# Optimization experiments

Measured on AMD Instinct MI355X. Metric: run time of the kernel, lower is better.

Reference implementation:

```python
import jax, jax.numpy as jnp
import numpy as np

N_NODES = 50000
N_EDGES = 800000
DIM = 64
N_HEADS = 4


def setup_inputs() -> dict:
    key = jax.random.key(0)
    ks = jax.random.split(key, 7)
    x = jax.random.normal(ks[0], (N_NODES, DIM), dtype=jnp.float32)
    Wq = jax.random.normal(ks[1], (DIM, DIM), dtype=jnp.float32) / np.sqrt(DIM)
    Wk = jax.random.normal(ks[2], (DIM, DIM), dtype=jnp.float32) / np.sqrt(DIM)
    Wv = jax.random.normal(ks[3], (DIM, DIM), dtype=jnp.float32) / np.sqrt(DIM)
    Wo = jax.random.normal(ks[4], (DIM, DIM), dtype=jnp.float32) / np.sqrt(DIM)
    src = jax.random.randint(ks[5], (N_EDGES,), 0, N_NODES, dtype=jnp.int32)
    dst = jax.random.randint(ks[6], (N_EDGES,), 0, N_NODES, dtype=jnp.int32)
    return {"x": x, "Wq": Wq, "Wk": Wk, "Wv": Wv, "Wo": Wo, "src": src, "dst": dst}


def _scatter_softmax(scores, dst, n_nodes):
    # scores: [E, H]; per-destination-node softmax over incoming edges.
    m = jax.ops.segment_max(scores, dst, num_segments=n_nodes)  # [N, H]
    m = jnp.maximum(m, jnp.float32(-1e9))  # mirror the -1e9 init of the torch code
    ex = jnp.exp(scores - m[dst])  # [E, H]
    denom = jax.ops.segment_sum(ex, dst, num_segments=n_nodes)  # [N, H]
    return ex / (denom[dst] + 1e-9)


def reference(x, Wq, Wk, Wv, Wo, src, dst):
    N, D = x.shape
    H = N_HEADS
    Dh = D // H
    q = (x @ Wq).reshape(N, H, Dh)
    k = (x @ Wk).reshape(N, H, Dh)
    v = (x @ Wv).reshape(N, H, Dh)
    # per-edge attention logits: [E, H]
    scores = jnp.einsum("ehd,ehd->eh", q[dst], k[src]) / jnp.sqrt(jnp.float32(Dh))
    alpha = _scatter_softmax(scores, dst, N)  # [E, H]
    # weighted aggregation of source values onto destination nodes
    agg = jax.ops.segment_sum(alpha[:, :, None] * v[src], dst, num_segments=N)  # [N, H, Dh]
    return agg.reshape(N, D) @ Wo
```

## Files before the change

### kernel.cpp

```cpp
#include <hip/hip_runtime.h>
#include <math.h>

#define HEADS 4
#define DH 16
#define D 64
#define MAXDEG 64

typedef unsigned short ushort_t;
typedef unsigned int uint_t;

__device__ __forceinline__ float bf2f(ushort_t u) {
    return __uint_as_float(((uint_t)u) << 16);
}
__device__ __forceinline__ ushort_t f2bf(float f) {
    uint_t u = __float_as_uint(f);
    u = (u + 0x7FFFu + ((u >> 16) & 1u)) >> 16;
    return (ushort_t)u;
}
__device__ __forceinline__ float bflo(uint_t u) { return __uint_as_float(u << 16); }
__device__ __forceinline__ float bfhi(uint_t u) { return __uint_as_float(u & 0xFFFF0000u); }

__global__ __launch_bounds__(256) void scatter_qkv_kernel(
        const float* __restrict__ x,
        const float* __restrict__ Wq,
        const float* __restrict__ Wk,
        const float* __restrict__ Wv,
        ushort_t* __restrict__ qbf,
        ushort_t* __restrict__ kbf,
        ushort_t* __restrict__ vbf,
        const int* __restrict__ src,
        const int* __restrict__ dst,
        int* __restrict__ cursor,
        ushort_t* __restrict__ csr,
        int N, int E) {
    __shared__ ushort_t wq[D][D];
    __shared__ ushort_t wk[D][D];
    __shared__ ushort_t wv[D][D];
    __shared__ float xs[16][D];

    int tid = threadIdx.x;

    {
        int e0 = (int)((long long)E * blockIdx.x / gridDim.x);
        int e1 = (int)((long long)E * (blockIdx.x + 1) / gridDim.x);
        for (int e = e0 + tid; e < e1; e += 256) {
            int d = dst[e];
            int s = src[e];
            int pos = atomicAdd(&cursor[d], 1);
            if (pos < MAXDEG) csr[(size_t)d * MAXDEG + pos] = (ushort_t)s;
        }
    }

    for (int i = tid; i < D * D; i += 256) {
        wq[i >> 6][i & 63] = f2bf(Wq[i]);
        wk[i >> 6][i & 63] = f2bf(Wk[i]);
        wv[i >> 6][i & 63] = f2bf(Wv[i]);
    }

    int c = tid & 63;
    int g = tid >> 6;
    int row = tid >> 4;
    int col4 = tid & 15;

    int ntiles = (N + 15) >> 4;
    for (int tile = blockIdx.x; tile < ntiles; tile += gridDim.x) {
        int n0t = tile * 16;
        __syncthreads();
        float4 xv = make_float4(0.f, 0.f, 0.f, 0.f);
        if (n0t + row < N) xv = *(const float4*)(x + (size_t)(n0t + row) * D + col4 * 4);
        *(float4*)&xs[row][col4 * 4] = xv;
        __syncthreads();

        float aq0=0,aq1=0,aq2=0,aq3=0, ak0=0,ak1=0,ak2=0,ak3=0, av0=0,av1=0,av2=0,av3=0;
#pragma unroll 8
        for (int d = 0; d < D; ++d) {
            float wqv = bf2f(wq[d][c]), wkv = bf2f(wk[d][c]), wvv = bf2f(wv[d][c]);
            float x0 = xs[g*4+0][d], x1 = xs[g*4+1][d], x2 = xs[g*4+2][d], x3 = xs[g*4+3][d];
            aq0 += x0*wqv; ak0 += x0*wkv; av0 += x0*wvv;
            aq1 += x1*wqv; ak1 += x1*wkv; av1 += x1*wvv;
            aq2 += x2*wqv; ak2 += x2*wkv; av2 += x2*wvv;
            aq3 += x3*wqv; ak3 += x3*wkv; av3 += x3*wvv;
        }
        int nb = n0t + g * 4;
        if (nb+0 < N) { qbf[(size_t)(nb+0)*D+c]=f2bf(aq0); kbf[(size_t)(nb+0)*D+c]=f2bf(ak0); vbf[(size_t)(nb+0)*D+c]=f2bf(av0); }
        if (nb+1 < N) { qbf[(size_t)(nb+1)*D+c]=f2bf(aq1); kbf[(size_t)(nb+1)*D+c]=f2bf(ak1); vbf[(size_t)(nb+1)*D+c]=f2bf(av1); }
        if (nb+2 < N) { qbf[(size_t)(nb+2)*D+c]=f2bf(aq2); kbf[(size_t)(nb+2)*D+c]=f2bf(ak2); vbf[(size_t)(nb+2)*D+c]=f2bf(av2); }
        if (nb+3 < N) { qbf[(size_t)(nb+3)*D+c]=f2bf(aq3); kbf[(size_t)(nb+3)*D+c]=f2bf(ak3); vbf[(size_t)(nb+3)*D+c]=f2bf(av3); }
    }
}

__global__ __launch_bounds__(512) void attn_kernel(const ushort_t* __restrict__ qbf,
                                                   const ushort_t* __restrict__ kbf,
                                                   const ushort_t* __restrict__ vbf,
                                                   const ushort_t* __restrict__ csr,
                                                   const int* __restrict__ cursor,
                                                   const float* __restrict__ Wo,
                                                   float* __restrict__ out,
                                                   int N) {
    __shared__ float wo[D][D];
    __shared__ float aggsh[8][D];

    int tid = threadIdx.x;
    for (int i = tid; i < D * D; i += 512) wo[i >> 6][i & 63] = Wo[i];
    __syncthreads();

    int lane = tid & 63;
    int wave = tid >> 6;
    int node = blockIdx.x * 8 + wave;
    if (node >= N) return;

    int hp  = lane & 3;
    int el  = lane >> 2;
    int hd  = (lane & 31) >> 3;
    int par = lane >> 5;
    int dp2 = 2 * (lane & 31);

    int cnt = cursor[node]; if (cnt > MAXDEG) cnt = MAXDEG;
    const ushort_t* row = csr + (size_t)node * MAXDEG;

    float qr[16];
    {
        const uint4* qp = (const uint4*)(qbf + (size_t)node * D + hp * DH);
        uint4 qa = qp[0], qb = qp[1];
        qr[0]=bflo(qa.x);  qr[1]=bfhi(qa.x);  qr[2]=bflo(qa.y);  qr[3]=bfhi(qa.y);
        qr[4]=bflo(qa.z);  qr[5]=bfhi(qa.z);  qr[6]=bflo(qa.w);  qr[7]=bfhi(qa.w);
        qr[8]=bflo(qb.x);  qr[9]=bfhi(qb.x);  qr[10]=bflo(qb.y); qr[11]=bfhi(qb.y);
        qr[12]=bflo(qb.z); qr[13]=bfhi(qb.z); qr[14]=bflo(qb.w); qr[15]=bfhi(qb.w);
    }

    int s0=0, s1=0, s2=0, s3=0;
    float sc0=-1e30f, sc1=-1e30f, sc2=-1e30f, sc3=-1e30f;

#define PH1SB(sb, sv, scv)                                                      \
    if ((sb) * 16 < cnt) {                                                      \
        int eidx = (sb) * 16 + el;                                              \
        if (eidx < cnt) sv = row[eidx];                                         \
        const uint4* kp = (const uint4*)(kbf + (size_t)sv * D + hp * DH);       \
        uint4 ka = kp[0], kb = kp[1];                                           \
        float dot =                                                             \
          bflo(ka.x)*qr[0]  + bfhi(ka.x)*qr[1]                                  \
        + bflo(ka.y)*qr[2]  + bfhi(ka.y)*qr[3]                                  \
        + bflo(ka.z)*qr[4]  + bfhi(ka.z)*qr[5]                                  \
        + bflo(ka.w)*qr[6]  + bfhi(ka.w)*qr[7]                                  \
        + bflo(kb.x)*qr[8]  + bfhi(kb.x)*qr[9]                                  \
        + bflo(kb.y)*qr[10] + bfhi(kb.y)*qr[11]                                 \
        + bflo(kb.z)*qr[12] + bfhi(kb.z)*qr[13]                                 \
        + bflo(kb.w)*qr[14] + bfhi(kb.w)*qr[15];                                \
        scv = (eidx < cnt) ? dot * 0.25f : -1e30f;                              \
    }
    PH1SB(0, s0, sc0)
    PH1SB(1, s1, sc1)
    PH1SB(2, s2, sc2)
    PH1SB(3, s3, sc3)
#undef PH1SB

    float mloc = fmaxf(fmaxf(sc0, sc1), fmaxf(sc2, sc3));
    mloc = fmaxf(mloc, __shfl_xor(mloc, 4, 64));
    mloc = fmaxf(mloc, __shfl_xor(mloc, 8, 64));
    mloc = fmaxf(mloc, __shfl_xor(mloc, 16, 64));
    mloc = fmaxf(mloc, __shfl_xor(mloc, 32, 64));
    mloc = fmaxf(mloc, -1e9f);

    float pv0 = __expf(sc0 - mloc);
    float pv1 = __expf(sc1 - mloc);
    float pv2 = __expf(sc2 - mloc);
    float pv3 = __expf(sc3 - mloc);
    float ls = (pv0 + pv1) + (pv2 + pv3);
    ls += __shfl_xor(ls, 4, 64);
    ls += __shfl_xor(ls, 8, 64);
    ls += __shfl_xor(ls, 16, 64);
    ls += __shfl_xor(ls, 32, 64);

    float inv = 1.f / (__shfl(ls, hd, 64) + 1e-9f);

    float2 a0 = {0.f, 0.f}, a1 = {0.f, 0.f};
#define PH3SB(sb, sv, pvv)                                                      \
    if ((sb) * 16 < cnt) {                                                      \
        int lim = cnt - (sb) * 16; if (lim > 16) lim = 16;                      \
        for (int e2 = 0; e2 < lim; e2 += 4) {                                   \
            int L0 = 4 * (e2 + par);                                            \
            int ss0 = __shfl(sv, L0, 64);                                       \
            float p0 = __shfl(pvv, L0 + hd, 64);                                \
            uint_t w0 = *(const uint_t*)(vbf + (size_t)ss0 * D + dp2);          \
            a0.x += p0 * bflo(w0);                                              \
            a0.y += p0 * bfhi(w0);                                              \
            int L1 = 4 * (e2 + 2 + par);                                        \
            int ss1 = __shfl(sv, L1, 64);                                       \
            float p1 = __shfl(pvv, L1 + hd, 64);                                \
            uint_t w1 = *(const uint_t*)(vbf + (size_t)ss1 * D + dp2);          \
            a1.x += p1 * bflo(w1);                                              \
            a1.y += p1 * bfhi(w1);                                              \
        }                                                                       \
    }
    PH3SB(0, s0, pv0)
    PH3SB(1, s1, pv1)
    PH3SB(2, s2, pv2)
    PH3SB(3, s3, pv3)
#undef PH3SB

    float ax = a0.x + a1.x, ay = a0.y + a1.y;
    ax += __shfl_xor(ax, 32, 64);
    ay += __shfl_xor(ay, 32, 64);
    if (lane < 32) {
        aggsh[wave][dp2]     = ax * inv;
        aggsh[wave][dp2 + 1] = ay * inv;
    }

    float o = 0.f;
#pragma unroll 8
    for (int d = 0; d < D; ++d) {
        o += aggsh[wave][d] * wo[d][lane];
    }
    out[(size_t)node * D + lane] = o;
}

extern "C" void kernel_launch(void* const* d_in, const int* in_sizes, int n_in,
                              void* d_out, int out_size, void* d_ws, size_t ws_size,
                              hipStream_t stream) {
    const float* x  = (const float*)d_in[0];
    const float* Wq = (const float*)d_in[1];
    const float* Wk = (const float*)d_in[2];
    const float* Wv = (const float*)d_in[3];
    const float* Wo = (const float*)d_in[4];
    const int* src  = (const int*)d_in[5];
    const int* dst  = (const int*)d_in[6];
    float* out = (float*)d_out;

    int N = in_sizes[0] / D;
    int E = in_sizes[5];

    char* ws = (char*)d_ws;
    ushort_t* qbf   = (ushort_t*)ws;  ws += (size_t)N * D * 2;
    ushort_t* kbf   = (ushort_t*)ws;  ws += (size_t)N * D * 2;
    ushort_t* vbf   = (ushort_t*)ws;  ws += (size_t)N * D * 2;
    int* cursor     = (int*)ws;       ws += (size_t)N * 4;
    ushort_t* csr   = (ushort_t*)ws;  ws += (size_t)N * MAXDEG * 2;

    int attnGrid = (N + 7) / 8;

    hipMemsetAsync(cursor, 0, (size_t)N * 4, stream);
    scatter_qkv_kernel<<<2048, 256, 0, stream>>>(x, Wq, Wk, Wv, qbf, kbf, vbf,
                                                 src, dst, cursor, csr, N, E);
    attn_kernel<<<attnGrid, 512, 0, stream>>>(qbf, kbf, vbf, csr, cursor, Wo, out, N);
}
```

Baseline: 121.9 us.

## Replace global-atomic CSR build with two-pass shared-memory bucketed scatter

The fused scatter+QKV kernel is split into three kernels. A bucketing pass partitions edges by destination range into 256 coarse buckets using shared-memory atomics and writes them out in 16-byte chunks. The QKV GEMM then runs on its own, and a second pass builds the per-node CSR with shared-memory counters per bucket. This removes the 800K random global atomics on the cursor array and the memset of that array. In exchange it adds two kernel launches and an extra round trip of packed edges through memory. It also relies on spill and bucket-capacity limits that could silently drop edges in overflow cases, and on 16-bit packing of node indices.

```diff
diff --git a/kernel.cpp b/kernel.cpp
--- a/kernel.cpp
+++ b/kernel.cpp
@@ -5,6 +5,10 @@
 #define DH 16
 #define D 64
 #define MAXDEG 64
+#define NB2 256
+#define BCAP 16
+#define SPILLCAP 8192
+#define SENTINEL 0xFFFFFFFFu
 
 typedef unsigned short ushort_t;
 typedef unsigned int uint_t;
@@ -20,37 +24,68 @@
 __device__ __forceinline__ float bflo(uint_t u) { return __uint_as_float(u << 16); }
 __device__ __forceinline__ float bfhi(uint_t u) { return __uint_as_float(u & 0xFFFF0000u); }
 
-__global__ __launch_bounds__(256) void scatter_qkv_kernel(
-        const float* __restrict__ x,
-        const float* __restrict__ Wq,
-        const float* __restrict__ Wk,
-        const float* __restrict__ Wv,
-        ushort_t* __restrict__ qbf,
-        ushort_t* __restrict__ kbf,
-        ushort_t* __restrict__ vbf,
-        const int* __restrict__ src,
-        const int* __restrict__ dst,
-        int* __restrict__ cursor,
-        ushort_t* __restrict__ csr,
-        int N, int E) {
+__global__ __launch_bounds__(256) void bucket_kernel(const int* __restrict__ src,
+                                                     const int* __restrict__ dst,
+                                                     int* __restrict__ gcur,
+                                                     uint_t* __restrict__ gbkt,
+                                                     uint_t* __restrict__ gspill,
+                                                     int E, int cap, int npb) {
+    __shared__ __align__(16) uint_t bbuf[NB2][BCAP];
+    __shared__ int bcnt[NB2];
+
+    int tid = threadIdx.x;
+    bcnt[tid] = 0;
+    __syncthreads();
+
+    int e0 = (int)((long long)E * blockIdx.x / gridDim.x);
+    int e1 = (int)((long long)E * (blockIdx.x + 1) / gridDim.x);
+    for (int e = e0 + tid; e < e1; e += 256) {
+        int d = dst[e];
+        int s = src[e];
+        int b = d / npb;
+        uint_t w = ((uint_t)d << 16) | (uint_t)s;
+        int p = atomicAdd(&bcnt[b], 1);
+        if (p < BCAP) {
+            bbuf[b][p] = w;
+        } else {
+            int gp = atomicAdd(&gcur[NB2], 1);
+            if (gp < SPILLCAP) gspill[gp] = w;
+        }
+    }
+    __syncthreads();
+
+    int cnt = bcnt[tid]; if (cnt > BCAP) cnt = BCAP;
+    int pad = (cnt + 3) & ~3;
+    for (int i = cnt; i < pad; ++i) bbuf[tid][i] = SENTINEL;
+    if (pad > 0) {
+        int base = atomicAdd(&gcur[tid], pad);
+        if (base + pad <= cap) {
+            uint_t* dp = gbkt + (size_t)tid * cap + base;
+            for (int i = 0; i < pad; i += 4)
+                *(uint4*)(dp + i) = *(const uint4*)&bbuf[tid][i];
+        } else {
+            for (int i = 0; i < cnt; ++i) {
+                int gp = atomicAdd(&gcur[NB2], 1);
+                if (gp < SPILLCAP) gspill[gp] = bbuf[tid][i];
+            }
+        }
+    }
+}
+
+__global__ __launch_bounds__(256) void qkv_kernel(const float* __restrict__ x,
+                                                  const float* __restrict__ Wq,
+                                                  const float* __restrict__ Wk,
+                                                  const float* __restrict__ Wv,
+                                                  ushort_t* __restrict__ qbf,
+                                                  ushort_t* __restrict__ kbf,
+                                                  ushort_t* __restrict__ vbf,
+                                                  int N) {
     __shared__ ushort_t wq[D][D];
     __shared__ ushort_t wk[D][D];
     __shared__ ushort_t wv[D][D];
     __shared__ float xs[16][D];
 
     int tid = threadIdx.x;
-
-    {
-        int e0 = (int)((long long)E * blockIdx.x / gridDim.x);
-        int e1 = (int)((long long)E * (blockIdx.x + 1) / gridDim.x);
-        for (int e = e0 + tid; e < e1; e += 256) {
-            int d = dst[e];
-            int s = src[e];
-            int pos = atomicAdd(&cursor[d], 1);
-            if (pos < MAXDEG) csr[(size_t)d * MAXDEG + pos] = (ushort_t)s;
-        }
-    }
-
     for (int i = tid; i < D * D; i += 256) {
         wq[i >> 6][i & 63] = f2bf(Wq[i]);
         wk[i >> 6][i & 63] = f2bf(Wk[i]);
@@ -86,6 +121,51 @@
         if (nb+1 < N) { qbf[(size_t)(nb+1)*D+c]=f2bf(aq1); kbf[(size_t)(nb+1)*D+c]=f2bf(ak1); vbf[(size_t)(nb+1)*D+c]=f2bf(av1); }
         if (nb+2 < N) { qbf[(size_t)(nb+2)*D+c]=f2bf(aq2); kbf[(size_t)(nb+2)*D+c]=f2bf(ak2); vbf[(size_t)(nb+2)*D+c]=f2bf(av2); }
         if (nb+3 < N) { qbf[(size_t)(nb+3)*D+c]=f2bf(aq3); kbf[(size_t)(nb+3)*D+c]=f2bf(ak3); vbf[(size_t)(nb+3)*D+c]=f2bf(av3); }
+    }
+}
+
+__global__ __launch_bounds__(256) void scatter2_kernel(const uint_t* __restrict__ gbkt,
+                                                       const uint_t* __restrict__ gspill,
+                                                       const int* __restrict__ gcur,
+                                                       int* __restrict__ cursor,
+                                                       ushort_t* __restrict__ csr,
+                                                       int N, int cap, int npb) {
+    __shared__ int cnt[NB2];
+
+    int tid = threadIdx.x;
+    int p = blockIdx.x;
+    int lo = p * npb;
+    int hi = lo + npb; if (hi > N) hi = N;
+
+    cnt[tid] = 0;
+    __syncthreads();
+
+    if (lo < N) {
+        int bc = gcur[p]; if (bc > cap) bc = cap;
+        const uint_t* bkt = gbkt + (size_t)p * cap;
+        for (int i = tid; i < bc; i += 256) {
+            uint_t w = bkt[i];
+            if (w == SENTINEL) continue;
+            int d = (int)(w >> 16);
+            int pos = atomicAdd(&cnt[d - lo], 1);
+            if (pos < MAXDEG) csr[(size_t)d * MAXDEG + pos] = (ushort_t)(w & 0xFFFFu);
+        }
+        int sc = gcur[NB2]; if (sc > SPILLCAP) sc = SPILLCAP;
+        for (int i = tid; i < sc; i += 256) {
+            uint_t w = gspill[i];
+            int d = (int)(w >> 16);
+            if (d >= lo && d < hi) {
+                int pos = atomicAdd(&cnt[d - lo], 1);
+                if (pos < MAXDEG) csr[(size_t)d * MAXDEG + pos] = (ushort_t)(w & 0xFFFFu);
+            }
+        }
+    }
+    __syncthreads();
+
+    int node = lo + tid;
+    if (tid < npb && node < N) {
+        int c = cnt[tid]; if (c > MAXDEG) c = MAXDEG;
+        cursor[node] = c;
     }
 }
 
@@ -228,6 +308,8 @@
 
     int N = in_sizes[0] / D;
     int E = in_sizes[5];
+    int npb = (N + NB2 - 1) / NB2;
+    int cap = 8192;
 
     char* ws = (char*)d_ws;
     ushort_t* qbf   = (ushort_t*)ws;  ws += (size_t)N * D * 2;
@@ -235,11 +317,17 @@
     ushort_t* vbf   = (ushort_t*)ws;  ws += (size_t)N * D * 2;
     int* cursor     = (int*)ws;       ws += (size_t)N * 4;
     ushort_t* csr   = (ushort_t*)ws;  ws += (size_t)N * MAXDEG * 2;
-
+    int* gcur       = (int*)ws;       ws += 512 * 4;
+    uint_t* gspill  = (uint_t*)ws;    ws += (size_t)SPILLCAP * 4;
+    uint_t* gbkt    = (uint_t*)ws;    ws += (size_t)NB2 * cap * 4;
+
+    int nTiles16 = (N + 15) / 16;
+    int gemmGrid = nTiles16 < 2048 ? nTiles16 : 2048;
     int attnGrid = (N + 7) / 8;
 
-    hipMemsetAsync(cursor, 0, (size_t)N * 4, stream);
-    scatter_qkv_kernel<<<2048, 256, 0, stream>>>(x, Wq, Wk, Wv, qbf, kbf, vbf,
-                                                 src, dst, cursor, csr, N, E);
+    hipMemsetAsync(gcur, 0, 512 * 4, stream);
+    bucket_kernel<<<1024, 256, 0, stream>>>(src, dst, gcur, gbkt, gspill, E, cap, npb);
+    qkv_kernel<<<gemmGrid, 256, 0, stream>>>(x, Wq, Wk, Wv, qbf, kbf, vbf, N);
+    scatter2_kernel<<<NB2, 256, 0, stream>>>(gbkt, gspill, gcur, cursor, csr, N, cap, npb);
     attn_kernel<<<attnGrid, 512, 0, stream>>>(qbf, kbf, vbf, csr, cursor, Wo, out, N);
 }
```

New measurement: 127.9 us. 5.0% more time.
